# Performance work log

Hardware: AMD Instinct MI355X
Metric: run time of the kernel (lower is better)

The kernel has to match this reference:

```python
import jax, jax.numpy as jnp
import numpy as np

N = 100000   # num_nodes
D = 128      # input_dim
DO = 128     # output_dim
V = 3        # num_views/relations
E = 500000   # edges per view
C = 2        # num_classes
H = D // 2   # label-attention hidden
VH = DO // 2 # view-attention hidden
EPS = 1e-5


def setup_inputs() -> dict:
    key = jax.random.key(0)
    ks = jax.random.split(key, 20)
    s = 0.05
    def nrm(k, shape):
        return jax.random.normal(k, shape, dtype=jnp.float32) * s
    return {
        'features': jax.random.normal(ks[0], (N, D), dtype=jnp.float32),
        'edge_src': jax.random.randint(ks[1], (V, E), 0, N, dtype=jnp.int32),
        'edge_dst': jax.random.randint(ks[2], (V, E), 0, N, dtype=jnp.int32),
        'edge_w': jax.random.uniform(ks[3], (V, E), dtype=jnp.float32),
        'clsW': nrm(ks[4], (D, C)), 'clsb': jnp.zeros((C,), jnp.float32),
        'attW1': nrm(ks[5], (C, D, H)), 'attb1': jnp.zeros((C, H), jnp.float32),
        'attW2': nrm(ks[6], (C, H)), 'attb2': jnp.zeros((C,), jnp.float32),
        'att_bias': jnp.float32(0.1),
        'relW': nrm(ks[7], (V, D, DO)), 'relb': jnp.zeros((V, DO), jnp.float32),
        'gateW': nrm(ks[8], (V, DO, DO)), 'gateb': jnp.zeros((V, DO), jnp.float32),
        'view_pref': jax.random.normal(ks[9], (V, DO), dtype=jnp.float32),
        'vattW1': nrm(ks[10], (DO, VH)), 'vattb1': jnp.zeros((VH,), jnp.float32),
        'vattW2': nrm(ks[11], (VH,)), 'vattb2': jnp.float32(0.0),
        'selfW': nrm(ks[12], (D, DO)), 'selfb': jnp.zeros((DO,), jnp.float32),
        'featW': nrm(ks[13], (D, DO)), 'featb': jnp.zeros((DO,), jnp.float32),
        'fusW': nrm(ks[14], (2 * DO, DO)), 'fusb': jnp.zeros((DO,), jnp.float32),
        'ln_g': jnp.ones((DO,), jnp.float32), 'ln_b': jnp.zeros((DO,), jnp.float32),
    }


def reference(features, edge_src, edge_dst, edge_w,
              clsW, clsb, attW1, attb1, attW2, attb2, att_bias,
              relW, relb, gateW, gateb,
              view_pref, vattW1, vattb1, vattW2, vattb2,
              selfW, selfb, featW, featb, fusW, fusb, ln_g, ln_b):
    # --- LabelAwareAttention ---
    class_probs = jax.nn.softmax(features @ clsW + clsb, axis=-1)          # [N,C]
    h = jax.nn.relu(jnp.einsum('nd,cdh->cnh', features, attW1) + attb1[:, None, :])
    scores = jax.nn.sigmoid(jnp.einsum('cnh,ch->cn', h, attW2) + attb2[:, None])
    node_att = jnp.sum(scores.T * class_probs, axis=-1) + att_bias         # [N]

    # --- per-view RelationAggregator (num_relations=1 -> relation weight is 1) ---
    src_f = features[edge_src]                                             # [V,E,D]
    msg = (jnp.einsum('ved,vdo->veo', src_f, relW) + relb[:, None, :]) \
          * edge_w[..., None]                                              # [V,E,DO]
    agg = jax.vmap(lambda m, d: jax.ops.segment_sum(m, d, num_segments=N))(
        msg, edge_dst)                                                     # [V,N,DO]
    gate = jax.nn.sigmoid(jnp.einsum('vno,vop->vnp', agg, gateW) + gateb[:, None, :])
    view_out = gate * agg                                                  # [V,N,DO]

    # --- ViewLevelAttention ---
    vh = jax.nn.relu(jnp.einsum('vno,oh->vnh', view_out * view_pref[:, None, :], vattW1) + vattb1)
    vscores = jnp.einsum('vnh,h->vn', vh, vattW2) + vattb2                 # [V,N]
    vweights = jax.nn.softmax(vscores, axis=0)                             # softmax over views
    combined = jnp.sum(view_out * vweights[..., None], axis=0)             # [N,DO]

    # --- fusion + residual + layer norm (dropout=0, eval) ---
    self_out = features @ selfW + selfb
    transformed = features @ featW + featb
    weighted = combined * node_att[:, None]
    fused = jax.nn.relu(jnp.concatenate([self_out, weighted], axis=-1) @ fusW + fusb)
    out = fused + transformed
    mu = jnp.mean(out, axis=-1, keepdims=True)
    var = jnp.var(out, axis=-1, keepdims=True)
    out = (out - mu) / jnp.sqrt(var + EPS) * ln_g + ln_b
    return out, class_probs
```

## Files before the change

### kernel.cpp

```cpp
#include <hip/hip_runtime.h>
#include <hip/hip_bf16.h>

#define NN 100000
#define DD 128
#define VV 3
#define EE 500000
#define TOT (VV * NN)
#define NB ((TOT + 255) / 256)
#define RGB ((NN + 127) / 128)

typedef unsigned short u16;
typedef unsigned int u32;
typedef short s8v __attribute__((ext_vector_type(8)));
typedef float f4v __attribute__((ext_vector_type(4)));

__device__ __forceinline__ float bf2f(u16 u) {
    return __uint_as_float(((u32)u) << 16);
}
__device__ __forceinline__ u16 f2bf(float f) {
    u32 x = __float_as_uint(f);
    u32 r = (x + 0x7fffu + ((x >> 16) & 1u)) >> 16;
    return (u16)r;
}

__device__ __forceinline__ void atomAddBf16x2(u16* addr, float f0, float f1) {
#if __has_builtin(__builtin_amdgcn_global_atomic_fadd_v2bf16)
    typedef short v2s __attribute__((ext_vector_type(2)));
    typedef v2s __attribute__((address_space(1)))* v2s_gp;
    v2s v;
    v.x = (short)f2bf(f0);
    v.y = (short)f2bf(f1);
    __builtin_amdgcn_global_atomic_fadd_v2bf16((v2s_gp)(void*)addr, v);
#else
    u32* p = (u32*)addr;
    u32 old = *(volatile u32*)p;
    while (true) {
        float lo = bf2f((u16)(old & 0xffffu)) + f0;
        float hi = bf2f((u16)(old >> 16)) + f1;
        u32 nv = (u32)f2bf(lo) | ((u32)f2bf(hi) << 16);
        u32 prev = atomicCAS(p, old, nv);
        if (prev == old) break;
        old = prev;
    }
#endif
}

template<int XSTR, int WSTR>
__device__ __forceinline__ void gemm16(float acc[4][4], const float* Xs,
                                       const float* Ws, int n0, int o0, int kbase) {
    #pragma unroll 4
    for (int kk = 0; kk < 64; kk += 4) {
        float4 w0 = *reinterpret_cast<const float4*>(Ws + (kk + 0) * WSTR + o0);
        float4 w1 = *reinterpret_cast<const float4*>(Ws + (kk + 1) * WSTR + o0);
        float4 w2 = *reinterpret_cast<const float4*>(Ws + (kk + 2) * WSTR + o0);
        float4 w3 = *reinterpret_cast<const float4*>(Ws + (kk + 3) * WSTR + o0);
        #pragma unroll
        for (int i = 0; i < 4; ++i) {
            float4 x = *reinterpret_cast<const float4*>(Xs + (n0 + i) * XSTR + kbase + kk);
            acc[i][0] = fmaf(x.x, w0.x, fmaf(x.y, w1.x, fmaf(x.z, w2.x, fmaf(x.w, w3.x, acc[i][0]))));
            acc[i][1] = fmaf(x.x, w0.y, fmaf(x.y, w1.y, fmaf(x.z, w2.y, fmaf(x.w, w3.y, acc[i][1]))));
            acc[i][2] = fmaf(x.x, w0.z, fmaf(x.y, w1.z, fmaf(x.z, w2.z, fmaf(x.w, w3.z, acc[i][2]))));
            acc[i][3] = fmaf(x.x, w0.w, fmaf(x.y, w1.w, fmaf(x.z, w2.w, fmaf(x.w, w3.w, acc[i][3]))));
        }
    }
}

template<int WSTR, int NT>
__device__ __forceinline__ void stage_w_f32(float* Ws, const float* __restrict__ src, int tid) {
    #pragma unroll
    for (int rep = 0; rep < 2048 / NT; ++rep) {
        int flat = rep * NT + tid;
        int kk = flat >> 5;
        int c4 = flat & 31;
        float4 q = *reinterpret_cast<const float4*>(src + kk * 128 + c4 * 4);
        *reinterpret_cast<float4*>(Ws + kk * WSTR + c4 * 4) = q;
    }
}

template<int XSTR, int NT>
__device__ __forceinline__ void stage_x_f32(float* Xs, const float* __restrict__ src, int tid) {
    #pragma unroll
    for (int rep = 0; rep < 1024 / NT; ++rep) {
        int flat = rep * NT + tid;
        int n = flat >> 5;
        int c4 = flat & 31;
        float4 q = *reinterpret_cast<const float4*>(src + (size_t)n * 128 + c4 * 4);
        *reinterpret_cast<float4*>(Xs + n * XSTR + c4 * 4) = q;
    }
}

template<int XSTR, int NT>
__device__ __forceinline__ void stage_x_bf16(float* Xs, const u16* __restrict__ src, int tid) {
    #pragma unroll
    for (int rep = 0; rep < 512 / NT; ++rep) {
        int flat = rep * NT + tid;
        int n = flat >> 4;
        int c8 = flat & 15;
        uint4 q = *reinterpret_cast<const uint4*>(src + (size_t)n * 128 + c8 * 8);
        float* d = Xs + n * XSTR + c8 * 8;
        d[0] = bf2f((u16)(q.x & 0xffffu)); d[1] = bf2f((u16)(q.x >> 16));
        d[2] = bf2f((u16)(q.y & 0xffffu)); d[3] = bf2f((u16)(q.y >> 16));
        d[4] = bf2f((u16)(q.z & 0xffffu)); d[5] = bf2f((u16)(q.z >> 16));
        d[6] = bf2f((u16)(q.w & 0xffffu)); d[7] = bf2f((u16)(q.w >> 16));
    }
}

__global__ void prep_kernel(const float* __restrict__ selfW, const float* __restrict__ selfb,
                            const float* __restrict__ fusW, const float* __restrict__ fusb,
                            float* __restrict__ Wsf, float* __restrict__ c1) {
    int o = threadIdx.x;
    int k = blockIdx.x;
    if (k < 128) {
        float acc = 0.f;
        for (int m = 0; m < 128; ++m)
            acc += selfW[k * 128 + m] * fusW[m * 128 + o];
        Wsf[k * 128 + o] = acc;
    } else {
        float acc = 0.f;
        for (int m = 0; m < 128; ++m)
            acc += selfb[m] * fusW[m * 128 + o];
        c1[o] = acc + fusb[o];
    }
}

__global__ __launch_bounds__(128) void wprep_kernel(
        const float* __restrict__ relW, const float* __restrict__ gateW,
        u16* __restrict__ relWb, u16* __restrict__ gateWb) {
    int k = threadIdx.x;
    int n = blockIdx.x & 127;
    int v = blockIdx.x >> 7;
    size_t o = ((size_t)v * 128 + n) * 128 + k;
    size_t i = ((size_t)v * 128 + k) * 128 + n;
    relWb[o]  = f2bf(relW[i]);
    gateWb[o] = f2bf(gateW[i]);
}

__global__ __launch_bounds__(128) void wprep2_kernel(
        const float* __restrict__ Wsf, const float* __restrict__ featW,
        const float* __restrict__ fusW,
        u16* __restrict__ WsfB, u16* __restrict__ featWB, u16* __restrict__ fusWbB) {
    int k = threadIdx.x;
    int n = blockIdx.x;
    WsfB[n * 128 + k]   = f2bf(Wsf[k * 128 + n]);
    featWB[n * 128 + k] = f2bf(featW[k * 128 + n]);
    fusWbB[n * 128 + k] = f2bf(fusW[(size_t)(128 + k) * 128 + n]);
}

__global__ __launch_bounds__(128) void wprep3_kernel(
        const float* __restrict__ attW1, u16* __restrict__ attW1B) {
    int k = threadIdx.x;
    int o = blockIdx.x;
    int c = o >> 6, h = o & 63;
    attW1B[o * 128 + k] = f2bf(attW1[((size_t)c * 128 + k) * 64 + h]);
}

__global__ __launch_bounds__(256) void featconv_kernel(
        const float* __restrict__ feat, u16* __restrict__ featB) {
    int t = blockIdx.x * 256 + threadIdx.x;
    float4 q = *reinterpret_cast<const float4*>(feat + (size_t)t * 4);
    ushort4 r;
    r.x = f2bf(q.x); r.y = f2bf(q.y); r.z = f2bf(q.z); r.w = f2bf(q.w);
    *reinterpret_cast<ushort4*>(featB + (size_t)t * 4) = r;
}


__global__ __launch_bounds__(256) void count_kernel(
        const int* __restrict__ edst, int* __restrict__ C) {
    int t = blockIdx.x * 256 + threadIdx.x;
    if (t >= VV * EE) return;
    int v = t / EE;
    atomicAdd(&C[v * NN + edst[t]], 1);
}

__global__ __launch_bounds__(256) void scanA_kernel(
        const int* __restrict__ C, int* __restrict__ bs) {
    int b = blockIdx.x, t = threadIdx.x;
    int i = b * 256 + t;
    int v = (i < TOT) ? C[i] : 0;
    __shared__ int s[256];
    s[t] = v;
    __syncthreads();
    #pragma unroll
    for (int off = 128; off > 0; off >>= 1) {
        if (t < off) s[t] += s[t + off];
        __syncthreads();
    }
    if (t == 0) bs[b] = s[0];
}

__global__ __launch_bounds__(1024) void scanB_kernel(int* __restrict__ bs) {
    __shared__ int s[2048];
    int t = threadIdx.x;
    int v0 = (t < NB) ? bs[t] : 0;
    int v1 = (t + 1024 < NB) ? bs[t + 1024] : 0;
    s[t] = v0; s[t + 1024] = v1;
    __syncthreads();
    #pragma unroll
    for (int off = 1; off < 2048; off <<= 1) {
        int x0 = (t >= off) ? s[t - off] : 0;
        int x1 = (t + 1024 >= off) ? s[t + 1024 - off] : 0;
        __syncthreads();
        s[t] += x0; s[t + 1024] += x1;
        __syncthreads();
    }
    if (t < NB) bs[t] = s[t] - v0;
    if (t + 1024 < NB) bs[t + 1024] = s[t + 1024] - v1;
}

__global__ __launch_bounds__(256) void scanC_kernel(
        int* __restrict__ C, const int* __restrict__ bs) {
    int b = blockIdx.x, t = threadIdx.x;
    int i = b * 256 + t;
    int v = (i < TOT) ? C[i] : 0;
    __shared__ int s[256];
    s[t] = v;
    __syncthreads();
    #pragma unroll
    for (int off = 1; off < 256; off <<= 1) {
        int x = (t >= off) ? s[t - off] : 0;
        __syncthreads();
        s[t] += x;
        __syncthreads();
    }
    if (i < TOT) C[i] = s[t] - v + bs[b];
}

__global__ __launch_bounds__(256) void fill_kernel(
        const int* __restrict__ esrc, const int* __restrict__ edst,
        const float* __restrict__ ew, int* __restrict__ C,
        int2* __restrict__ bsw) {
    int t = blockIdx.x * 256 + threadIdx.x;
    if (t >= VV * EE) return;
    int v = t / EE;
    int pos = atomicAdd(&C[v * NN + edst[t]], 1);
    int2 p;
    p.x = esrc[t];
    p.y = __float_as_int(ew[t]);
    bsw[pos] = p;
}

__global__ __launch_bounds__(256) void gather_kernel(
        const u16* __restrict__ featB, const int* __restrict__ C,
        const int2* __restrict__ bsw,
        u16* __restrict__ aggB, float* __restrict__ wsum) {
    int wid = (blockIdx.x * 256 + threadIdx.x) >> 6;
    int lane = threadIdx.x & 63;
    int end = C[wid];
    int start = (wid == 0) ? 0 : C[wid - 1];
    float a0 = 0.f, a1 = 0.f, wacc = 0.f;
    int e = start;
    for (; e + 4 <= end; e += 4) {
        int2 p0 = bsw[e], p1 = bsw[e + 1], p2 = bsw[e + 2], p3 = bsw[e + 3];
        u32 f0 = *reinterpret_cast<const u32*>(featB + (size_t)p0.x * DD + lane * 2);
        u32 f1 = *reinterpret_cast<const u32*>(featB + (size_t)p1.x * DD + lane * 2);
        u32 f2 = *reinterpret_cast<const u32*>(featB + (size_t)p2.x * DD + lane * 2);
        u32 f3 = *reinterpret_cast<const u32*>(featB + (size_t)p3.x * DD + lane * 2);
        float w0 = __int_as_float(p0.y), w1 = __int_as_float(p1.y);
        float w2 = __int_as_float(p2.y), w3 = __int_as_float(p3.y);
        a0 = fmaf(w0, bf2f((u16)(f0 & 0xffffu)), a0);
        a1 = fmaf(w0, bf2f((u16)(f0 >> 16)), a1);
        a0 = fmaf(w1, bf2f((u16)(f1 & 0xffffu)), a0);
        a1 = fmaf(w1, bf2f((u16)(f1 >> 16)), a1);
        a0 = fmaf(w2, bf2f((u16)(f2 & 0xffffu)), a0);
        a1 = fmaf(w2, bf2f((u16)(f2 >> 16)), a1);
        a0 = fmaf(w3, bf2f((u16)(f3 & 0xffffu)), a0);
        a1 = fmaf(w3, bf2f((u16)(f3 >> 16)), a1);
        wacc += (w0 + w1) + (w2 + w3);
    }
    for (; e < end; ++e) {
        int2 p = bsw[e];
        float w = __int_as_float(p.y);
        u32 f = *reinterpret_cast<const u32*>(featB + (size_t)p.x * DD + lane * 2);
        a0 = fmaf(w, bf2f((u16)(f & 0xffffu)), a0);
        a1 = fmaf(w, bf2f((u16)(f >> 16)), a1);
        wacc += w;
    }
    u32 packed = (u32)f2bf(a0) | ((u32)f2bf(a1) << 16);
    *reinterpret_cast<u32*>(aggB + (size_t)wid * DD + lane * 2) = packed;
    if (lane == 0) wsum[wid] = wacc;
}

__global__ __launch_bounds__(256) void scatter_kernel(
        const int* __restrict__ esrc, const int* __restrict__ edst,
        const float* __restrict__ ew, const float* __restrict__ feat,
        u16* __restrict__ aggB, float* __restrict__ wsum) {
    long long t = (long long)blockIdx.x * 256 + threadIdx.x;
    int lane = (int)(t & 31);
    int eg = (int)(t >> 5);
    int v = eg / EE;
    int src = 0, dst = 0; float w = 0.f;
    if (lane == 0) {
        src = esrc[eg]; dst = edst[eg]; w = ew[eg];
    }
    src = __shfl(src, 0, 32);
    dst = __shfl(dst, 0, 32);
    w   = __shfl(w, 0, 32);
    const float* fr = feat + (size_t)src * DD + lane * 4;
    float4 q = *reinterpret_cast<const float4*>(fr);
    u16* outp = aggB + ((size_t)v * NN + dst) * DD + lane * 4;
    atomAddBf16x2(outp,     w * q.x, w * q.y);
    atomAddBf16x2(outp + 2, w * q.z, w * q.w);
    if (lane == 0) atomicAdd(wsum + v * NN + dst, w);
}

__global__ __launch_bounds__(256) void label_mfma_kernel(
        const u16* __restrict__ featB, const u16* __restrict__ attW1B,
        const float* __restrict__ clsW, const float* __restrict__ clsb,
        const float* __restrict__ attb1, const float* __restrict__ attW2,
        const float* __restrict__ attb2, const float* __restrict__ att_bias,
        float* __restrict__ node_att, float* __restrict__ probs_out) {
    __shared__ u16 Xs[128][136];
    __shared__ u16 Wt[128][72];
    int tid = threadIdx.x;
    int wv = tid >> 6, lane = tid & 63;
    int quad = lane >> 4, l15 = lane & 15;
    int row0 = blockIdx.x * 128;

    #pragma unroll
    for (int rep = 0; rep < 8; ++rep) {
        int flat = rep * 256 + tid;
        int n = flat >> 4, c8 = flat & 15;
        int gr = row0 + n; if (gr >= NN) gr = NN - 1;
        uint4 q = *reinterpret_cast<const uint4*>(featB + (size_t)gr * DD + c8 * 8);
        *reinterpret_cast<uint4*>(&Xs[n][c8 * 8]) = q;
    }

    f4v acc[2][8];
    #pragma unroll
    for (int rt = 0; rt < 2; ++rt)
        #pragma unroll
        for (int c = 0; c < 8; ++c)
            acc[rt][c] = f4v{0.f, 0.f, 0.f, 0.f};

    #pragma unroll
    for (int h = 0; h < 2; ++h) {
        #pragma unroll
        for (int rep = 0; rep < 4; ++rep) {
            int flat = rep * 256 + tid;
            int n = flat >> 3, c8 = flat & 7;
            uint4 q = *reinterpret_cast<const uint4*>(attW1B + (size_t)n * DD + h * 64 + c8 * 8);
            *reinterpret_cast<uint4*>(&Wt[n][c8 * 8]) = q;
        }
        __syncthreads();
        #pragma unroll
        for (int t = 0; t < 2; ++t) {
            int kl = t * 32 + quad * 8;
            s8v a0 = *reinterpret_cast<const s8v*>(&Xs[wv * 32 + l15][h * 64 + kl]);
            s8v a1 = *reinterpret_cast<const s8v*>(&Xs[wv * 32 + 16 + l15][h * 64 + kl]);
            #pragma unroll
            for (int c = 0; c < 8; ++c) {
                s8v b = *reinterpret_cast<const s8v*>(&Wt[c * 16 + l15][kl]);
                acc[0][c] = __builtin_amdgcn_mfma_f32_16x16x32_bf16(a0, b, acc[0][c], 0, 0, 0);
                acc[1][c] = __builtin_amdgcn_mfma_f32_16x16x32_bf16(a1, b, acc[1][c], 0, 0, 0);
            }
        }
        __syncthreads();
    }

    float ab1[8], aw2[8];
    #pragma unroll
    for (int c = 0; c < 8; ++c) {
        int col = c * 16 + l15;
        ab1[c] = attb1[col];
        aw2[c] = attW2[col];
    }
    float cw0[8], cw1[8];
    #pragma unroll
    for (int j = 0; j < 8; ++j) {
        int k = l15 * 8 + j;
        cw0[j] = clsW[k * 2];
        cw1[j] = clsW[k * 2 + 1];
    }
    float cb0 = clsb[0], cb1 = clsb[1];
    float b20 = attb2[0], b21 = attb2[1];
    float abias = att_bias[0];

    #pragma unroll
    for (int rt = 0; rt < 2; ++rt)
        #pragma unroll
        for (int r = 0; r < 4; ++r) {
            int n = wv * 32 + rt * 16 + quad * 4 + r;
            int gr = row0 + n;
            float p0 = 0.f, p1 = 0.f;
            #pragma unroll
            for (int c = 0; c < 4; ++c) {
                float hv = acc[rt][c][r] + ab1[c];
                hv = hv > 0.f ? hv : 0.f;
                p0 += hv * aw2[c];
            }
            #pragma unroll
            for (int c = 4; c < 8; ++c) {
                float hv = acc[rt][c][r] + ab1[c];
                hv = hv > 0.f ? hv : 0.f;
                p1 += hv * aw2[c];
            }
            uint4 q = *reinterpret_cast<const uint4*>(&Xs[n][l15 * 8]);
            float f[8];
            f[0] = bf2f((u16)(q.x & 0xffffu)); f[1] = bf2f((u16)(q.x >> 16));
            f[2] = bf2f((u16)(q.y & 0xffffu)); f[3] = bf2f((u16)(q.y >> 16));
            f[4] = bf2f((u16)(q.z & 0xffffu)); f[5] = bf2f((u16)(q.z >> 16));
            f[6] = bf2f((u16)(q.w & 0xffffu)); f[7] = bf2f((u16)(q.w >> 16));
            float l0 = 0.f, l1 = 0.f;
            #pragma unroll
            for (int j = 0; j < 8; ++j) {
                l0 = fmaf(f[j], cw0[j], l0);
                l1 = fmaf(f[j], cw1[j], l1);
            }
            #pragma unroll
            for (int m = 1; m < 16; m <<= 1) {
                p0 += __shfl_xor(p0, m);
                p1 += __shfl_xor(p1, m);
                l0 += __shfl_xor(l0, m);
                l1 += __shfl_xor(l1, m);
            }
            if (l15 == 0 && gr < NN) {
                float s0 = 1.f / (1.f + expf(-(p0 + b20)));
                float s1 = 1.f / (1.f + expf(-(p1 + b21)));
                l0 += cb0; l1 += cb1;
                float mm = fmaxf(l0, l1);
                float e0 = expf(l0 - mm), e1 = expf(l1 - mm);
                float inv = 1.f / (e0 + e1);
                float q0 = e0 * inv, q1 = e1 * inv;
                node_att[gr] = q0 * s0 + q1 * s1 + abias;
                probs_out[gr * 2]     = q0;
                probs_out[gr * 2 + 1] = q1;
            }
        }
}

__global__ __launch_bounds__(256) void label_kernel(
        const float* __restrict__ feat, const float* __restrict__ clsW, const float* __restrict__ clsb,
        const float* __restrict__ attW1, const float* __restrict__ attb1,
        const float* __restrict__ attW2, const float* __restrict__ attb2,
        const float* __restrict__ att_bias,
        float* __restrict__ node_att, float* __restrict__ probs_out) {
    __shared__ float Xs[32][132];
    __shared__ float Ws[64][132];
    int tid = threadIdx.x;
    int row0 = blockIdx.x * 32;
    stage_x_f32<132, 256>(&Xs[0][0], feat + (size_t)row0 * DD, tid);
    int to = tid & 31, tn = tid >> 5;
    int o0 = to * 4, n0 = tn * 4;
    float acc[4][4] = {};
    for (int half = 0; half < 2; ++half) {
        __syncthreads();
        #pragma unroll
        for (int rep = 0; rep < 8; ++rep) {
            int flat = rep * 256 + tid;
            int kk = flat >> 5, o4 = flat & 31;
            int o = o4 * 4;
            int c = o >> 6, h = o & 63;
            int k = half * 64 + kk;
            float4 q = *reinterpret_cast<const float4*>(attW1 + (size_t)(c * 128 + k) * 64 + h);
            *reinterpret_cast<float4*>(&Ws[kk][o]) = q;
        }
        __syncthreads();
        gemm16<132, 132>(acc, &Xs[0][0], &Ws[0][0], n0, o0, half * 64);
    }
    int c = o0 >> 6, h0 = o0 & 63;
    float b1j[4], w2j[4];
    #pragma unroll
    for (int j = 0; j < 4; ++j) {
        b1j[j] = attb1[c * 64 + h0 + j];
        w2j[j] = attW2[c * 64 + h0 + j];
    }
    float part[4];
    #pragma unroll
    for (int i = 0; i < 4; ++i) {
        float s = 0.f;
        #pragma unroll
        for (int j = 0; j < 4; ++j) {
            float hv = acc[i][j] + b1j[j];
            hv = hv > 0.f ? hv : 0.f;
            s += hv * w2j[j];
        }
        part[i] = s;
    }
    __syncthreads();
    float* red = &Ws[0][0];
    float* Ssc = red + 32 * 33;
    float* Lsc = Ssc + 64;
    #pragma unroll
    for (int i = 0; i < 4; ++i) red[(n0 + i) * 33 + to] = part[i];
    __syncthreads();
    if (tid < 64) {
        int n = tid >> 1, cc = tid & 1;
        float l = 0.f;
        for (int k = 0; k < 128; k += 4) {
            float4 x = *reinterpret_cast<const float4*>(&Xs[n][k]);
            l += x.x * clsW[(k + 0) * 2 + cc];
            l += x.y * clsW[(k + 1) * 2 + cc];
            l += x.z * clsW[(k + 2) * 2 + cc];
            l += x.w * clsW[(k + 3) * 2 + cc];
        }
        Lsc[n * 2 + cc] = l + clsb[cc];
        float s = 0.f;
        for (int u = 0; u < 16; ++u) s += red[n * 33 + cc * 16 + u];
        s += attb2[cc];
        Ssc[n * 2 + cc] = 1.f / (1.f + expf(-s));
    }
    __syncthreads();
    if (tid < 32) {
        int n = tid;
        float l0 = Lsc[n * 2], l1 = Lsc[n * 2 + 1];
        float m = fmaxf(l0, l1);
        float e0 = expf(l0 - m), e1 = expf(l1 - m);
        float inv = 1.f / (e0 + e1);
        float p0 = e0 * inv, p1 = e1 * inv;
        float na = p0 * Ssc[n * 2] + p1 * Ssc[n * 2 + 1] + att_bias[0];
        int row = row0 + n;
        node_att[row] = na;
        probs_out[row * 2]     = p0;
        probs_out[row * 2 + 1] = p1;
    }
}

__global__ __launch_bounds__(256) void relgate_mfma_kernel(
        const u16* __restrict__ relWb, const float* __restrict__ relb,
        const u16* __restrict__ gateWb, const float* __restrict__ gateb,
        u16* __restrict__ aggB, const float* __restrict__ wsum) {
    __shared__ u16 Xs[128][136];
    __shared__ u16 Wt[128][72];
    int tid = threadIdx.x;
    int wv = tid >> 6, lane = tid & 63;
    int quad = lane >> 4, l15 = lane & 15;
    int v = blockIdx.y;
    int row0 = blockIdx.x * 128;
    const size_t vbase = (size_t)v * NN;

    #pragma unroll
    for (int rep = 0; rep < 8; ++rep) {
        int flat = rep * 256 + tid;
        int n = flat >> 4, c8 = flat & 15;
        int gr = row0 + n; if (gr >= NN) gr = NN - 1;
        uint4 q = *reinterpret_cast<const uint4*>(aggB + (vbase + gr) * DD + c8 * 8);
        *reinterpret_cast<uint4*>(&Xs[n][c8 * 8]) = q;
    }

    f4v acc1[2][8], acc2[2][8];
    #pragma unroll
    for (int rt = 0; rt < 2; ++rt)
        #pragma unroll
        for (int c = 0; c < 8; ++c) {
            acc1[rt][c] = f4v{0.f, 0.f, 0.f, 0.f};
            acc2[rt][c] = f4v{0.f, 0.f, 0.f, 0.f};
        }

    const u16* W1 = relWb + (size_t)v * DD * DD;
    const u16* W2 = gateWb + (size_t)v * DD * DD;

    #pragma unroll
    for (int h = 0; h < 2; ++h) {
        #pragma unroll
        for (int rep = 0; rep < 4; ++rep) {
            int flat = rep * 256 + tid;
            int n = flat >> 3, c8 = flat & 7;
            uint4 q = *reinterpret_cast<const uint4*>(W1 + (size_t)n * DD + h * 64 + c8 * 8);
            *reinterpret_cast<uint4*>(&Wt[n][c8 * 8]) = q;
        }
        __syncthreads();
        #pragma unroll
        for (int t = 0; t < 2; ++t) {
            int kl = t * 32 + quad * 8;
            s8v a0 = *reinterpret_cast<const s8v*>(&Xs[wv * 32 + l15][h * 64 + kl]);
            s8v a1 = *reinterpret_cast<const s8v*>(&Xs[wv * 32 + 16 + l15][h * 64 + kl]);
            #pragma unroll
            for (int c = 0; c < 8; ++c) {
                s8v b = *reinterpret_cast<const s8v*>(&Wt[c * 16 + l15][kl]);
                acc1[0][c] = __builtin_amdgcn_mfma_f32_16x16x32_bf16(a0, b, acc1[0][c], 0, 0, 0);
                acc1[1][c] = __builtin_amdgcn_mfma_f32_16x16x32_bf16(a1, b, acc1[1][c], 0, 0, 0);
            }
        }
        __syncthreads();
    }

    float wsn[2][4], rb[8];
    #pragma unroll
    for (int rt = 0; rt < 2; ++rt)
        #pragma unroll
        for (int r = 0; r < 4; ++r) {
            int gr = row0 + wv * 32 + rt * 16 + quad * 4 + r;
            wsn[rt][r] = wsum[vbase + (gr < NN ? gr : NN - 1)];
        }
    #pragma unroll
    for (int c = 0; c < 8; ++c) rb[c] = relb[v * DD + c * 16 + l15];
    #pragma unroll
    for (int rt = 0; rt < 2; ++rt)
        #pragma unroll
        for (int c = 0; c < 8; ++c)
            #pragma unroll
            for (int r = 0; r < 4; ++r)
                acc1[rt][c][r] += wsn[rt][r] * rb[c];

    #pragma unroll
    for (int rt = 0; rt < 2; ++rt)
        #pragma unroll
        for (int c = 0; c < 8; ++c)
            #pragma unroll
            for (int r = 0; r < 4; ++r)
                Xs[wv * 32 + rt * 16 + quad * 4 + r][c * 16 + l15] = f2bf(acc1[rt][c][r]);
    __syncthreads();

    #pragma unroll
    for (int h = 0; h < 2; ++h) {
        #pragma unroll
        for (int rep = 0; rep < 4; ++rep) {
            int flat = rep * 256 + tid;
            int n = flat >> 3, c8 = flat & 7;
            uint4 q = *reinterpret_cast<const uint4*>(W2 + (size_t)n * DD + h * 64 + c8 * 8);
            *reinterpret_cast<uint4*>(&Wt[n][c8 * 8]) = q;
        }
        __syncthreads();
        #pragma unroll
        for (int t = 0; t < 2; ++t) {
            int kl = t * 32 + quad * 8;
            s8v a0 = *reinterpret_cast<const s8v*>(&Xs[wv * 32 + l15][h * 64 + kl]);
            s8v a1 = *reinterpret_cast<const s8v*>(&Xs[wv * 32 + 16 + l15][h * 64 + kl]);
            #pragma unroll
            for (int c = 0; c < 8; ++c) {
                s8v b = *reinterpret_cast<const s8v*>(&Wt[c * 16 + l15][kl]);
                acc2[0][c] = __builtin_amdgcn_mfma_f32_16x16x32_bf16(a0, b, acc2[0][c], 0, 0, 0);
                acc2[1][c] = __builtin_amdgcn_mfma_f32_16x16x32_bf16(a1, b, acc2[1][c], 0, 0, 0);
            }
        }
        __syncthreads();
    }

    float gb[8];
    #pragma unroll
    for (int c = 0; c < 8; ++c) gb[c] = gateb[v * DD + c * 16 + l15];
    #pragma unroll
    for (int rt = 0; rt < 2; ++rt)
        #pragma unroll
        for (int c = 0; c < 8; ++c)
            #pragma unroll
            for (int r = 0; r < 4; ++r) {
                float g = 1.f / (1.f + expf(-(acc2[rt][c][r] + gb[c])));
                Xs[wv * 32 + rt * 16 + quad * 4 + r][c * 16 + l15] = f2bf(g * acc1[rt][c][r]);
            }
    __syncthreads();
    #pragma unroll
    for (int rep = 0; rep < 8; ++rep) {
        int flat = rep * 256 + tid;
        int n = flat >> 4, c8 = flat & 15;
        int gr = row0 + n;
        if (gr < NN)
            *reinterpret_cast<uint4*>(aggB + (vbase + gr) * DD + c8 * 8) =
                *reinterpret_cast<const uint4*>(&Xs[n][c8 * 8]);
    }
}

__global__ __launch_bounds__(256) void relgate_kernel(
        const float* __restrict__ relW, const float* __restrict__ relb,
        const float* __restrict__ gateW, const float* __restrict__ gateb,
        u16* __restrict__ aggB, const float* __restrict__ wsum) {
    __shared__ float Xs[32][128];
    __shared__ float Ws[64][132];
    int tid = threadIdx.x;
    int v = blockIdx.y;
    int row0 = blockIdx.x * 32;
    u16* base = aggB + ((size_t)v * NN + row0) * DD;
    stage_x_bf16<128, 256>(&Xs[0][0], base, tid);
    int to = tid & 31, tn = tid >> 5;
    int o0 = to * 4, n0 = tn * 4;
    float acc[4][4] = {};
    const float* W1 = relW + (size_t)v * DD * DD;
    for (int half = 0; half < 2; ++half) {
        __syncthreads();
        stage_w_f32<132, 256>(&Ws[0][0], W1 + half * 64 * DD, tid);
        __syncthreads();
        gemm16<128, 132>(acc, &Xs[0][0], &Ws[0][0], n0, o0, half * 64);
    }
    float wsn[4], rb[4];
    #pragma unroll
    for (int i = 0; i < 4; ++i) wsn[i] = wsum[v * NN + row0 + n0 + i];
    #pragma unroll
    for (int j = 0; j < 4; ++j) rb[j] = relb[v * DD + o0 + j];
    #pragma unroll
    for (int i = 0; i < 4; ++i)
        #pragma unroll
        for (int j = 0; j < 4; ++j) acc[i][j] += wsn[i] * rb[j];
    __syncthreads();
    #pragma unroll
    for (int i = 0; i < 4; ++i)
        *reinterpret_cast<float4*>(&Xs[n0 + i][o0]) = make_float4(acc[i][0], acc[i][1], acc[i][2], acc[i][3]);
    float acc2[4][4] = {};
    const float* W2 = gateW + (size_t)v * DD * DD;
    for (int half = 0; half < 2; ++half) {
        __syncthreads();
        stage_w_f32<132, 256>(&Ws[0][0], W2 + half * 64 * DD, tid);
        __syncthreads();
        gemm16<128, 132>(acc2, &Xs[0][0], &Ws[0][0], n0, o0, half * 64);
    }
    float gb[4];
    #pragma unroll
    for (int j = 0; j < 4; ++j) gb[j] = gateb[v * DD + o0 + j];
    #pragma unroll
    for (int i = 0; i < 4; ++i) {
        float g0 = 1.f / (1.f + expf(-(acc2[i][0] + gb[0])));
        float g1 = 1.f / (1.f + expf(-(acc2[i][1] + gb[1])));
        float g2 = 1.f / (1.f + expf(-(acc2[i][2] + gb[2])));
        float g3 = 1.f / (1.f + expf(-(acc2[i][3] + gb[3])));
        ushort4 r;
        r.x = f2bf(g0 * acc[i][0]); r.y = f2bf(g1 * acc[i][1]);
        r.z = f2bf(g2 * acc[i][2]); r.w = f2bf(g3 * acc[i][3]);
        *reinterpret_cast<ushort4*>(base + (size_t)(n0 + i) * DD + o0) = r;
    }
}

__global__ __launch_bounds__(128) void vatt_kernel(
        const u16* __restrict__ aggB, const float* __restrict__ view_pref,
        const float* __restrict__ vattW1, const float* __restrict__ vattb1,
        const float* __restrict__ vattW2, const float* __restrict__ vattb2,
        float* __restrict__ vscores) {
    __shared__ float Xs[32][132];
    __shared__ float Ws[128][68];
    int tid = threadIdx.x;
    int v = blockIdx.y;
    int row0 = blockIdx.x * 32;
    const u16* base = aggB + ((size_t)v * NN + row0) * DD;
    #pragma unroll
    for (int rep = 0; rep < 4; ++rep) {
        int flat = rep * 128 + tid;
        int n = flat >> 4, c8 = flat & 15;
        uint4 q = *reinterpret_cast<const uint4*>(base + (size_t)n * DD + c8 * 8);
        float4 pa = *reinterpret_cast<const float4*>(view_pref + v * DD + c8 * 8);
        float4 pb = *reinterpret_cast<const float4*>(view_pref + v * DD + c8 * 8 + 4);
        float* d = &Xs[n][c8 * 8];
        d[0] = bf2f((u16)(q.x & 0xffffu)) * pa.x; d[1] = bf2f((u16)(q.x >> 16)) * pa.y;
        d[2] = bf2f((u16)(q.y & 0xffffu)) * pa.z; d[3] = bf2f((u16)(q.y >> 16)) * pa.w;
        d[4] = bf2f((u16)(q.z & 0xffffu)) * pb.x; d[5] = bf2f((u16)(q.z >> 16)) * pb.y;
        d[6] = bf2f((u16)(q.w & 0xffffu)) * pb.z; d[7] = bf2f((u16)(q.w >> 16)) * pb.w;
    }
    #pragma unroll
    for (int rep = 0; rep < 16; ++rep) {
        int flat = rep * 128 + tid;
        int k = flat >> 4, c4 = flat & 15;
        float4 q = *reinterpret_cast<const float4*>(vattW1 + k * 64 + c4 * 4);
        *reinterpret_cast<float4*>(&Ws[k][c4 * 4]) = q;
    }
    __syncthreads();
    int to = tid & 15, tn = tid >> 4;
    int o0 = to * 4, n0 = tn * 4;
    float acc[4][4] = {};
    gemm16<132, 68>(acc, &Xs[0][0], &Ws[0][0], n0, o0, 0);
    gemm16<132, 68>(acc, &Xs[0][0], &Ws[64][0], n0, o0, 64);
    float b1[4], w2[4];
    #pragma unroll
    for (int j = 0; j < 4; ++j) {
        b1[j] = vattb1[o0 + j];
        w2[j] = vattW2[o0 + j];
    }
    float part[4];
    #pragma unroll
    for (int i = 0; i < 4; ++i) {
        float s = 0.f;
        #pragma unroll
        for (int j = 0; j < 4; ++j) {
            float hv = acc[i][j] + b1[j];
            hv = hv > 0.f ? hv : 0.f;
            s += hv * w2[j];
        }
        part[i] = s;
    }
    __syncthreads();
    float* red = &Ws[0][0];
    #pragma unroll
    for (int i = 0; i < 4; ++i) red[(n0 + i) * 17 + to] = part[i];
    __syncthreads();
    if (tid < 32) {
        float s = 0.f;
        for (int u = 0; u < 16; ++u) s += red[tid * 17 + u];
        vscores[(size_t)v * NN + row0 + tid] = s + vattb2[0];
    }
}

__global__ __launch_bounds__(256) void combine_kernel(
        u16* __restrict__ aggB, const float* __restrict__ vscores,
        const float* __restrict__ node_att) {
    int t = blockIdx.x * 256 + threadIdx.x;
    int n = t >> 5, c4 = t & 31;
    float s0 = vscores[n], s1 = vscores[NN + n], s2 = vscores[2 * NN + n];
    float m = fmaxf(s0, fmaxf(s1, s2));
    float e0 = expf(s0 - m), e1 = expf(s1 - m), e2 = expf(s2 - m);
    float inv = 1.f / (e0 + e1 + e2);
    float w0 = e0 * inv, w1 = e1 * inv, w2 = e2 * inv;
    float na = node_att[n];
    size_t off = (size_t)n * DD + c4 * 4;
    ushort4 q0 = *reinterpret_cast<const ushort4*>(aggB + off);
    ushort4 q1 = *reinterpret_cast<const ushort4*>(aggB + (size_t)NN * DD + off);
    ushort4 q2 = *reinterpret_cast<const ushort4*>(aggB + 2 * (size_t)NN * DD + off);
    ushort4 r;
    r.x = f2bf((bf2f(q0.x) * w0 + bf2f(q1.x) * w1 + bf2f(q2.x) * w2) * na);
    r.y = f2bf((bf2f(q0.y) * w0 + bf2f(q1.y) * w1 + bf2f(q2.y) * w2) * na);
    r.z = f2bf((bf2f(q0.z) * w0 + bf2f(q1.z) * w1 + bf2f(q2.z) * w2) * na);
    r.w = f2bf((bf2f(q0.w) * w0 + bf2f(q1.w) * w1 + bf2f(q2.w) * w2) * na);
    *reinterpret_cast<ushort4*>(aggB + off) = r;
}

__global__ __launch_bounds__(256) void final_mfma_kernel(
        const u16* __restrict__ featB, const u16* __restrict__ weightedB,
        const u16* __restrict__ WsfB, const u16* __restrict__ featWB,
        const u16* __restrict__ fusWbB,
        const float* __restrict__ c1, const float* __restrict__ featb,
        const float* __restrict__ ln_g, const float* __restrict__ ln_b,
        float* __restrict__ outp) {
    __shared__ u16 Xs[128][136];
    __shared__ u16 Wt[128][72];
    int tid = threadIdx.x;
    int wv = tid >> 6, lane = tid & 63;
    int quad = lane >> 4, l15 = lane & 15;
    int row0 = blockIdx.x * 128;

    #pragma unroll
    for (int rep = 0; rep < 8; ++rep) {
        int flat = rep * 256 + tid;
        int n = flat >> 4, c8 = flat & 15;
        int gr = row0 + n; if (gr >= NN) gr = NN - 1;
        uint4 q = *reinterpret_cast<const uint4*>(featB + (size_t)gr * DD + c8 * 8);
        *reinterpret_cast<uint4*>(&Xs[n][c8 * 8]) = q;
    }

    f4v acc1[2][8], acc2[2][8];
    #pragma unroll
    for (int rt = 0; rt < 2; ++rt)
        #pragma unroll
        for (int c = 0; c < 8; ++c) {
            acc1[rt][c] = f4v{0.f, 0.f, 0.f, 0.f};
            acc2[rt][c] = f4v{0.f, 0.f, 0.f, 0.f};
        }

    #pragma unroll
    for (int h = 0; h < 2; ++h) {
        #pragma unroll
        for (int rep = 0; rep < 4; ++rep) {
            int flat = rep * 256 + tid;
            int n = flat >> 3, c8 = flat & 7;
            uint4 q = *reinterpret_cast<const uint4*>(WsfB + (size_t)n * DD + h * 64 + c8 * 8);
            *reinterpret_cast<uint4*>(&Wt[n][c8 * 8]) = q;
        }
        __syncthreads();
        #pragma unroll
        for (int t = 0; t < 2; ++t) {
            int kl = t * 32 + quad * 8;
            s8v a0 = *reinterpret_cast<const s8v*>(&Xs[wv * 32 + l15][h * 64 + kl]);
            s8v a1 = *reinterpret_cast<const s8v*>(&Xs[wv * 32 + 16 + l15][h * 64 + kl]);
            #pragma unroll
            for (int c = 0; c < 8; ++c) {
                s8v b = *reinterpret_cast<const s8v*>(&Wt[c * 16 + l15][kl]);
                acc1[0][c] = __builtin_amdgcn_mfma_f32_16x16x32_bf16(a0, b, acc1[0][c], 0, 0, 0);
                acc1[1][c] = __builtin_amdgcn_mfma_f32_16x16x32_bf16(a1, b, acc1[1][c], 0, 0, 0);
            }
        }
        __syncthreads();
        #pragma unroll
        for (int rep = 0; rep < 4; ++rep) {
            int flat = rep * 256 + tid;
            int n = flat >> 3, c8 = flat & 7;
            uint4 q = *reinterpret_cast<const uint4*>(featWB + (size_t)n * DD + h * 64 + c8 * 8);
            *reinterpret_cast<uint4*>(&Wt[n][c8 * 8]) = q;
        }
        __syncthreads();
        #pragma unroll
        for (int t = 0; t < 2; ++t) {
            int kl = t * 32 + quad * 8;
            s8v a0 = *reinterpret_cast<const s8v*>(&Xs[wv * 32 + l15][h * 64 + kl]);
            s8v a1 = *reinterpret_cast<const s8v*>(&Xs[wv * 32 + 16 + l15][h * 64 + kl]);
            #pragma unroll
            for (int c = 0; c < 8; ++c) {
                s8v b = *reinterpret_cast<const s8v*>(&Wt[c * 16 + l15][kl]);
                acc2[0][c] = __builtin_amdgcn_mfma_f32_16x16x32_bf16(a0, b, acc2[0][c], 0, 0, 0);
                acc2[1][c] = __builtin_amdgcn_mfma_f32_16x16x32_bf16(a1, b, acc2[1][c], 0, 0, 0);
            }
        }
        __syncthreads();
    }

    #pragma unroll
    for (int rep = 0; rep < 8; ++rep) {
        int flat = rep * 256 + tid;
        int n = flat >> 4, c8 = flat & 15;
        int gr = row0 + n; if (gr >= NN) gr = NN - 1;
        uint4 q = *reinterpret_cast<const uint4*>(weightedB + (size_t)gr * DD + c8 * 8);
        *reinterpret_cast<uint4*>(&Xs[n][c8 * 8]) = q;
    }
    #pragma unroll
    for (int h = 0; h < 2; ++h) {
        #pragma unroll
        for (int rep = 0; rep < 4; ++rep) {
            int flat = rep * 256 + tid;
            int n = flat >> 3, c8 = flat & 7;
            uint4 q = *reinterpret_cast<const uint4*>(fusWbB + (size_t)n * DD + h * 64 + c8 * 8);
            *reinterpret_cast<uint4*>(&Wt[n][c8 * 8]) = q;
        }
        __syncthreads();
        #pragma unroll
        for (int t = 0; t < 2; ++t) {
            int kl = t * 32 + quad * 8;
            s8v a0 = *reinterpret_cast<const s8v*>(&Xs[wv * 32 + l15][h * 64 + kl]);
            s8v a1 = *reinterpret_cast<const s8v*>(&Xs[wv * 32 + 16 + l15][h * 64 + kl]);
            #pragma unroll
            for (int c = 0; c < 8; ++c) {
                s8v b = *reinterpret_cast<const s8v*>(&Wt[c * 16 + l15][kl]);
                acc1[0][c] = __builtin_amdgcn_mfma_f32_16x16x32_bf16(a0, b, acc1[0][c], 0, 0, 0);
                acc1[1][c] = __builtin_amdgcn_mfma_f32_16x16x32_bf16(a1, b, acc1[1][c], 0, 0, 0);
            }
        }
        __syncthreads();
    }

    float c1j[8], fbj[8], gj[8], bj[8];
    #pragma unroll
    for (int c = 0; c < 8; ++c) {
        int col = c * 16 + l15;
        c1j[c] = c1[col];
        fbj[c] = featb[col];
        gj[c]  = ln_g[col];
        bj[c]  = ln_b[col];
    }
    #pragma unroll
    for (int rt = 0; rt < 2; ++rt)
        #pragma unroll
        for (int c = 0; c < 8; ++c)
            #pragma unroll
            for (int r = 0; r < 4; ++r) {
                float f = acc1[rt][c][r] + c1j[c];
                f = f > 0.f ? f : 0.f;
                acc1[rt][c][r] = f + acc2[rt][c][r] + fbj[c];
            }
    #pragma unroll
    for (int rt = 0; rt < 2; ++rt)
        #pragma unroll
        for (int r = 0; r < 4; ++r) {
            float s = 0.f, q = 0.f;
            #pragma unroll
            for (int c = 0; c < 8; ++c) {
                float x = acc1[rt][c][r];
                s += x; q += x * x;
            }
            #pragma unroll
            for (int m = 1; m < 16; m <<= 1) {
                s += __shfl_xor(s, m);
                q += __shfl_xor(q, m);
            }
            float mu = s * (1.f / 128.f);
            float var = q * (1.f / 128.f) - mu * mu;
            float rs = rsqrtf(var + 1e-5f);
            int gr = row0 + wv * 32 + rt * 16 + quad * 4 + r;
            if (gr < NN) {
                #pragma unroll
                for (int c = 0; c < 8; ++c)
                    outp[(size_t)gr * DD + c * 16 + l15] =
                        (acc1[rt][c][r] - mu) * rs * gj[c] + bj[c];
            }
        }
}

__global__ __launch_bounds__(256) void final_kernel(
        const float* __restrict__ feat, const u16* __restrict__ weightedB,
        const float* __restrict__ Wsf, const float* __restrict__ c1,
        const float* __restrict__ fusW, const float* __restrict__ featW,
        const float* __restrict__ featb, const float* __restrict__ ln_g,
        const float* __restrict__ ln_b, float* __restrict__ outp) {
    __shared__ float Xs[32][128];
    __shared__ float Ws[64][128];
    int tid = threadIdx.x;
    int row0 = blockIdx.x * 32;
    stage_x_f32<128, 256>(&Xs[0][0], feat + (size_t)row0 * DD, tid);
    int to = tid & 31, tn = tid >> 5;
    int o0 = to * 4, n0 = tn * 4;
    float acc1[4][4] = {}, acc2[4][4] = {};
    for (int half = 0; half < 2; ++half) {
        __syncthreads();
        stage_w_f32<128, 256>(&Ws[0][0], Wsf + half * 64 * 128, tid);
        __syncthreads();
        gemm16<128, 128>(acc1, &Xs[0][0], &Ws[0][0], n0, o0, half * 64);
    }
    for (int half = 0; half < 2; ++half) {
        __syncthreads();
        stage_w_f32<128, 256>(&Ws[0][0], featW + half * 64 * 128, tid);
        __syncthreads();
        gemm16<128, 128>(acc2, &Xs[0][0], &Ws[0][0], n0, o0, half * 64);
    }
    __syncthreads();
    stage_x_bf16<128, 256>(&Xs[0][0], weightedB + (size_t)row0 * DD, tid);
    for (int half = 0; half < 2; ++half) {
        __syncthreads();
        stage_w_f32<128, 256>(&Ws[0][0], fusW + (size_t)(128 + half * 64) * 128, tid);
        __syncthreads();
        gemm16<128, 128>(acc1, &Xs[0][0], &Ws[0][0], n0, o0, half * 64);
    }
    float c1j[4], fbj[4], gj[4], bj[4];
    #pragma unroll
    for (int j = 0; j < 4; ++j) {
        c1j[j] = c1[o0 + j];
        fbj[j] = featb[o0 + j];
        gj[j]  = ln_g[o0 + j];
        bj[j]  = ln_b[o0 + j];
    }
    float val[4][4];
    #pragma unroll
    for (int i = 0; i < 4; ++i)
        #pragma unroll
        for (int j = 0; j < 4; ++j) {
            float f = acc1[i][j] + c1j[j];
            f = f > 0.f ? f : 0.f;
            val[i][j] = f + acc2[i][j] + fbj[j];
        }
    __syncthreads();
    float* red_s = &Ws[0][0];
    float* red_q = red_s + 32 * 33;
    float* mus   = red_q + 32 * 33;
    float* rss   = mus + 32;
    #pragma unroll
    for (int i = 0; i < 4; ++i) {
        float s = 0.f, q = 0.f;
        #pragma unroll
        for (int j = 0; j < 4; ++j) { s += val[i][j]; q += val[i][j] * val[i][j]; }
        red_s[(n0 + i) * 33 + to] = s;
        red_q[(n0 + i) * 33 + to] = q;
    }
    __syncthreads();
    if (tid < 32) {
        float s = 0.f, q = 0.f;
        for (int u = 0; u < 32; ++u) { s += red_s[tid * 33 + u]; q += red_q[tid * 33 + u]; }
        float mu = s / 128.f;
        float var = q / 128.f - mu * mu;
        mus[tid] = mu;
        rss[tid] = rsqrtf(var + 1e-5f);
    }
    __syncthreads();
    #pragma unroll
    for (int i = 0; i < 4; ++i) {
        float mu = mus[n0 + i], rs = rss[n0 + i];
        float4 o;
        o.x = (val[i][0] - mu) * rs * gj[0] + bj[0];
        o.y = (val[i][1] - mu) * rs * gj[1] + bj[1];
        o.z = (val[i][2] - mu) * rs * gj[2] + bj[2];
        o.w = (val[i][3] - mu) * rs * gj[3] + bj[3];
        *reinterpret_cast<float4*>(outp + (size_t)(row0 + n0 + i) * DD + o0) = o;
    }
}

extern "C" void kernel_launch(void* const* d_in, const int* in_sizes, int n_in,
                              void* d_out, int out_size, void* d_ws, size_t ws_size,
                              hipStream_t stream) {
    (void)in_sizes; (void)n_in; (void)out_size;
    const float* feat      = (const float*)d_in[0];
    const int*   esrc      = (const int*)d_in[1];
    const int*   edst      = (const int*)d_in[2];
    const float* ew        = (const float*)d_in[3];
    const float* clsW      = (const float*)d_in[4];
    const float* clsb      = (const float*)d_in[5];
    const float* attW1     = (const float*)d_in[6];
    const float* attb1     = (const float*)d_in[7];
    const float* attW2     = (const float*)d_in[8];
    const float* attb2     = (const float*)d_in[9];
    const float* att_bias  = (const float*)d_in[10];
    const float* relW      = (const float*)d_in[11];
    const float* relb      = (const float*)d_in[12];
    const float* gateW     = (const float*)d_in[13];
    const float* gateb     = (const float*)d_in[14];
    const float* view_pref = (const float*)d_in[15];
    const float* vattW1    = (const float*)d_in[16];
    const float* vattb1    = (const float*)d_in[17];
    const float* vattW2    = (const float*)d_in[18];
    const float* vattb2    = (const float*)d_in[19];
    const float* selfW     = (const float*)d_in[20];
    const float* selfb     = (const float*)d_in[21];
    const float* featW     = (const float*)d_in[22];
    const float* featb     = (const float*)d_in[23];
    const float* fusW      = (const float*)d_in[24];
    const float* fusb      = (const float*)d_in[25];
    const float* ln_g      = (const float*)d_in[26];
    const float* ln_b      = (const float*)d_in[27];

    u16*   aggB = (u16*)d_ws;
    float* wsum = (float*)(aggB + (size_t)VV * NN * DD);
    float* natt = wsum + (size_t)VV * NN;
    float* vsc  = natt + NN;
    float* Wsf  = vsc + (size_t)VV * NN;
    float* c1   = Wsf + DD * DD;
    u16* relWb  = (u16*)(c1 + DD);
    u16* gateWb = relWb + (size_t)VV * DD * DD;
    u16* WsfB   = gateWb + (size_t)VV * DD * DD;
    u16* featWB = WsfB + DD * DD;
    u16* fusWbB = featWB + DD * DD;
    u16* attW1B = fusWbB + DD * DD;
    int*   C    = (int*)(attW1B + DD * DD);
    int*   bs   = C + (size_t)TOT;
    int2*  bsw  = (int2*)(bs + NB + 1);
    u16* featB  = (u16*)(bsw + (size_t)VV * EE);
    size_t needed = (size_t)((char*)(featB + (size_t)NN * DD) - (char*)d_ws);

    float* outp  = (float*)d_out;
    float* probs = outp + (size_t)NN * DD;

    prep_kernel<<<129, 128, 0, stream>>>(selfW, selfb, fusW, fusb, Wsf, c1);
    if (ws_size >= needed) {
        featconv_kernel<<<12500, 256, 0, stream>>>(feat, featB);
        wprep_kernel<<<384, 128, 0, stream>>>(relW, gateW, relWb, gateWb);
        wprep2_kernel<<<128, 128, 0, stream>>>(Wsf, featW, fusW, WsfB, featWB, fusWbB);
        wprep3_kernel<<<128, 128, 0, stream>>>(attW1, attW1B);
        label_mfma_kernel<<<RGB, 256, 0, stream>>>(featB, attW1B, clsW, clsb, attb1,
                                                   attW2, attb2, att_bias, natt, probs);
        hipMemsetAsync(C, 0, (size_t)TOT * sizeof(int), stream);
        count_kernel<<<(VV * EE + 255) / 256, 256, 0, stream>>>(edst, C);
        scanA_kernel<<<NB, 256, 0, stream>>>(C, bs);
        scanB_kernel<<<1, 1024, 0, stream>>>(bs);
        scanC_kernel<<<NB, 256, 0, stream>>>(C, bs);
        fill_kernel<<<(VV * EE + 255) / 256, 256, 0, stream>>>(esrc, edst, ew, C, bsw);
        gather_kernel<<<(VV * NN) / 4, 256, 0, stream>>>(featB, C, bsw, aggB, wsum);
        relgate_mfma_kernel<<<dim3(RGB, 3), 256, 0, stream>>>(relWb, relb, gateWb, gateb,
                                                              aggB, wsum);
        vatt_kernel<<<dim3(3125, 3), 128, 0, stream>>>(aggB, view_pref, vattW1, vattb1,
                                                       vattW2, vattb2, vsc);
        combine_kernel<<<12500, 256, 0, stream>>>(aggB, vsc, natt);
        final_mfma_kernel<<<RGB, 256, 0, stream>>>(featB, aggB, WsfB, featWB, fusWbB,
                                                   c1, featb, ln_g, ln_b, outp);
    } else {
        label_kernel<<<3125, 256, 0, stream>>>(feat, clsW, clsb, attW1, attb1, attW2, attb2,
                                               att_bias, natt, probs);
        hipMemsetAsync(d_ws, 0,
                       (size_t)VV * NN * DD * sizeof(u16) + (size_t)VV * NN * sizeof(float),
                       stream);
        scatter_kernel<<<187500, 256, 0, stream>>>(esrc, edst, ew, feat, aggB, wsum);
        relgate_kernel<<<dim3(3125, 3), 256, 0, stream>>>(relW, relb, gateW, gateb, aggB, wsum);
        vatt_kernel<<<dim3(3125, 3), 128, 0, stream>>>(aggB, view_pref, vattW1, vattb1,
                                                       vattW2, vattb2, vsc);
        combine_kernel<<<12500, 256, 0, stream>>>(aggB, vsc, natt);
        final_kernel<<<3125, 256, 0, stream>>>(feat, aggB, Wsf, c1, fusW, featW, featb,
                                               ln_g, ln_b, outp);
    }
}
```

Baseline: 722.1 us.

## Fuse view attention into relgate and view combine into final kernel

```diff
diff --git a/kernel.cpp b/kernel.cpp
--- a/kernel.cpp
+++ b/kernel.cpp
@@ -152,6 +152,16 @@
     int o = blockIdx.x;
     int c = o >> 6, h = o & 63;
     attW1B[o * 128 + k] = f2bf(attW1[((size_t)c * 128 + k) * 64 + h]);
+}
+
+__global__ __launch_bounds__(128) void wprep4_kernel(
+        const float* __restrict__ vattW1, const float* __restrict__ view_pref,
+        u16* __restrict__ vattW1p) {
+    int k = threadIdx.x;
+    int h = blockIdx.x & 63;
+    int v = blockIdx.x >> 6;
+    vattW1p[((size_t)v * 64 + h) * 128 + k] =
+        f2bf(view_pref[v * 128 + k] * vattW1[k * 64 + h]);
 }
 
 __global__ __launch_bounds__(256) void featconv_kernel(
@@ -518,7 +528,10 @@
 __global__ __launch_bounds__(256) void relgate_mfma_kernel(
         const u16* __restrict__ relWb, const float* __restrict__ relb,
         const u16* __restrict__ gateWb, const float* __restrict__ gateb,
-        u16* __restrict__ aggB, const float* __restrict__ wsum) {
+        const u16* __restrict__ vattW1p, const float* __restrict__ vattb1,
+        const float* __restrict__ vattW2, const float* __restrict__ vattb2,
+        u16* __restrict__ aggB, const float* __restrict__ wsum,
+        float* __restrict__ vscores) {
     __shared__ u16 Xs[128][136];
     __shared__ u16 Wt[128][72];
     int tid = threadIdx.x;
@@ -638,7 +651,20 @@
                 float g = 1.f / (1.f + expf(-(acc2[rt][c][r] + gb[c])));
                 Xs[wv * 32 + rt * 16 + quad * 4 + r][c * 16 + l15] = f2bf(g * acc1[rt][c][r]);
             }
-    __syncthreads();
+
+    {
+        const u16* Wv = vattW1p + (size_t)v * 64 * DD;
+        #pragma unroll
+        for (int rep = 0; rep < 4; ++rep) {
+            int flat = rep * 256 + tid;
+            int n = flat >> 4, c8 = flat & 15;
+            uint4 q = *reinterpret_cast<const uint4*>(Wv + (size_t)n * DD + c8 * 8);
+            int half = c8 >> 3;
+            *reinterpret_cast<uint4*>(&Wt[half * 64 + n][(c8 & 7) * 8]) = q;
+        }
+    }
+    __syncthreads();
+
     #pragma unroll
     for (int rep = 0; rep < 8; ++rep) {
         int flat = rep * 256 + tid;
@@ -648,6 +674,54 @@
             *reinterpret_cast<uint4*>(aggB + (vbase + gr) * DD + c8 * 8) =
                 *reinterpret_cast<const uint4*>(&Xs[n][c8 * 8]);
     }
+
+    f4v acc3[2][4];
+    #pragma unroll
+    for (int rt = 0; rt < 2; ++rt)
+        #pragma unroll
+        for (int c = 0; c < 4; ++c)
+            acc3[rt][c] = f4v{0.f, 0.f, 0.f, 0.f};
+    #pragma unroll
+    for (int h = 0; h < 2; ++h) {
+        #pragma unroll
+        for (int t = 0; t < 2; ++t) {
+            int kl = t * 32 + quad * 8;
+            s8v a0 = *reinterpret_cast<const s8v*>(&Xs[wv * 32 + l15][h * 64 + kl]);
+            s8v a1 = *reinterpret_cast<const s8v*>(&Xs[wv * 32 + 16 + l15][h * 64 + kl]);
+            #pragma unroll
+            for (int c = 0; c < 4; ++c) {
+                s8v b = *reinterpret_cast<const s8v*>(&Wt[h * 64 + c * 16 + l15][kl]);
+                acc3[0][c] = __builtin_amdgcn_mfma_f32_16x16x32_bf16(a0, b, acc3[0][c], 0, 0, 0);
+                acc3[1][c] = __builtin_amdgcn_mfma_f32_16x16x32_bf16(a1, b, acc3[1][c], 0, 0, 0);
+            }
+        }
+    }
+    float vb1[4], vw2[4];
+    #pragma unroll
+    for (int c = 0; c < 4; ++c) {
+        int col = c * 16 + l15;
+        vb1[c] = vattb1[col];
+        vw2[c] = vattW2[col];
+    }
+    float vb2 = vattb2[0];
+    #pragma unroll
+    for (int rt = 0; rt < 2; ++rt)
+        #pragma unroll
+        for (int r = 0; r < 4; ++r) {
+            float p = 0.f;
+            #pragma unroll
+            for (int c = 0; c < 4; ++c) {
+                float hv = acc3[rt][c][r] + vb1[c];
+                hv = hv > 0.f ? hv : 0.f;
+                p += hv * vw2[c];
+            }
+            #pragma unroll
+            for (int m = 1; m < 16; m <<= 1)
+                p += __shfl_xor(p, m);
+            int gr = row0 + wv * 32 + rt * 16 + quad * 4 + r;
+            if (l15 == 0 && gr < NN)
+                vscores[vbase + gr] = p + vb2;
+        }
 }
 
 __global__ __launch_bounds__(256) void relgate_kernel(
@@ -799,7 +873,8 @@
 }
 
 __global__ __launch_bounds__(256) void final_mfma_kernel(
-        const u16* __restrict__ featB, const u16* __restrict__ weightedB,
+        const u16* __restrict__ featB, const u16* __restrict__ aggB,
+        const float* __restrict__ vsc, const float* __restrict__ natt,
         const u16* __restrict__ WsfB, const u16* __restrict__ featWB,
         const u16* __restrict__ fusWbB,
         const float* __restrict__ c1, const float* __restrict__ featb,
@@ -807,6 +882,7 @@
         float* __restrict__ outp) {
     __shared__ u16 Xs[128][136];
     __shared__ u16 Wt[128][72];
+    __shared__ float rw[3][128];
     int tid = threadIdx.x;
     int wv = tid >> 6, lane = tid & 63;
     int quad = lane >> 4, l15 = lane & 15;
@@ -820,6 +896,17 @@
         uint4 q = *reinterpret_cast<const uint4*>(featB + (size_t)gr * DD + c8 * 8);
         *reinterpret_cast<uint4*>(&Xs[n][c8 * 8]) = q;
     }
+    if (tid < 128) {
+        int gr = row0 + tid; if (gr >= NN) gr = NN - 1;
+        float s0 = vsc[gr], s1 = vsc[NN + gr], s2 = vsc[2 * NN + gr];
+        float m = fmaxf(s0, fmaxf(s1, s2));
+        float e0 = expf(s0 - m), e1 = expf(s1 - m), e2 = expf(s2 - m);
+        float inv = 1.f / (e0 + e1 + e2);
+        float na = natt[gr];
+        rw[0][tid] = e0 * inv * na;
+        rw[1][tid] = e1 * inv * na;
+        rw[2][tid] = e2 * inv * na;
+    }
 
     f4v acc1[2][8], acc2[2][8];
     #pragma unroll
@@ -881,8 +968,23 @@
         int flat = rep * 256 + tid;
         int n = flat >> 4, c8 = flat & 15;
         int gr = row0 + n; if (gr >= NN) gr = NN - 1;
-        uint4 q = *reinterpret_cast<const uint4*>(weightedB + (size_t)gr * DD + c8 * 8);
-        *reinterpret_cast<uint4*>(&Xs[n][c8 * 8]) = q;
+        size_t off = (size_t)gr * DD + c8 * 8;
+        uint4 q0 = *reinterpret_cast<const uint4*>(aggB + off);
+        uint4 q1 = *reinterpret_cast<const uint4*>(aggB + (size_t)NN * DD + off);
+        uint4 q2 = *reinterpret_cast<const uint4*>(aggB + 2 * (size_t)NN * DD + off);
+        float w0 = rw[0][n], w1 = rw[1][n], w2 = rw[2][n];
+        u32 o[4];
+        const u32* a = &q0.x; const u32* b = &q1.x; const u32* c = &q2.x;
+        #pragma unroll
+        for (int j = 0; j < 4; ++j) {
+            float lo = bf2f((u16)(a[j] & 0xffffu)) * w0 + bf2f((u16)(b[j] & 0xffffu)) * w1
+                     + bf2f((u16)(c[j] & 0xffffu)) * w2;
+            float hi = bf2f((u16)(a[j] >> 16)) * w0 + bf2f((u16)(b[j] >> 16)) * w1
+                     + bf2f((u16)(c[j] >> 16)) * w2;
+            o[j] = (u32)f2bf(lo) | ((u32)f2bf(hi) << 16);
+        }
+        uint4 r; r.x = o[0]; r.y = o[1]; r.z = o[2]; r.w = o[3];
+        *reinterpret_cast<uint4*>(&Xs[n][c8 * 8]) = r;
     }
     #pragma unroll
     for (int h = 0; h < 2; ++h) {
@@ -1087,7 +1189,8 @@
     u16* featWB = WsfB + DD * DD;
     u16* fusWbB = featWB + DD * DD;
     u16* attW1B = fusWbB + DD * DD;
-    int*   C    = (int*)(attW1B + DD * DD);
+    u16* vattW1p = attW1B + DD * DD;
+    int*   C    = (int*)(vattW1p + (size_t)VV * 64 * DD);
     int*   bs   = C + (size_t)TOT;
     int2*  bsw  = (int2*)(bs + NB + 1);
     u16* featB  = (u16*)(bsw + (size_t)VV * EE);
@@ -1102,6 +1205,7 @@
         wprep_kernel<<<384, 128, 0, stream>>>(relW, gateW, relWb, gateWb);
         wprep2_kernel<<<128, 128, 0, stream>>>(Wsf, featW, fusW, WsfB, featWB, fusWbB);
         wprep3_kernel<<<128, 128, 0, stream>>>(attW1, attW1B);
+        wprep4_kernel<<<192, 128, 0, stream>>>(vattW1, view_pref, vattW1p);
         label_mfma_kernel<<<RGB, 256, 0, stream>>>(featB, attW1B, clsW, clsb, attb1,
                                                    attW2, attb2, att_bias, natt, probs);
         hipMemsetAsync(C, 0, (size_t)TOT * sizeof(int), stream);
@@ -1112,11 +1216,10 @@
         fill_kernel<<<(VV * EE + 255) / 256, 256, 0, stream>>>(esrc, edst, ew, C, bsw);
         gather_kernel<<<(VV * NN) / 4, 256, 0, stream>>>(featB, C, bsw, aggB, wsum);
         relgate_mfma_kernel<<<dim3(RGB, 3), 256, 0, stream>>>(relWb, relb, gateWb, gateb,
-                                                              aggB, wsum);
-        vatt_kernel<<<dim3(3125, 3), 128, 0, stream>>>(aggB, view_pref, vattW1, vattb1,
-                                                       vattW2, vattb2, vsc);
-        combine_kernel<<<12500, 256, 0, stream>>>(aggB, vsc, natt);
-        final_mfma_kernel<<<RGB, 256, 0, stream>>>(featB, aggB, WsfB, featWB, fusWbB,
+                                                              vattW1p, vattb1, vattW2, vattb2,
+                                                              aggB, wsum, vsc);
+        final_mfma_kernel<<<RGB, 256, 0, stream>>>(featB, aggB, vsc, natt,
+                                                   WsfB, featWB, fusWbB,
                                                    c1, featb, ln_g, ln_b, outp);
     } else {
         label_kernel<<<3125, 256, 0, stream>>>(feat, clsW, clsb, attW1, attb1, attW2, attb2,
```

New measurement: 674.0 us. 6.7% less time.
